# Optimization experiments

Hardware: AMD Instinct MI355X
Metric: run time of the kernel (lower is better)

The kernel has to match this reference:

```python
import jax, jax.numpy as jnp
import numpy as np

SCALE = 4
KUP = 5


def conv2d(x, w, b, pad=0):
    # x: (B,C,H,W), w: (O,I,kh,kw)
    y = jax.lax.conv_general_dilated(x, w, (1, 1), [(pad, pad), (pad, pad)],
                                     dimension_numbers=('NCHW', 'OIHW', 'NCHW'))
    return y + b[None, :, None, None]


def unfold(x, k):
    # torch F.unfold equivalent: (B,C,H,W) -> (B,C,k*k,H,W), channel-major patch order
    p = jax.lax.conv_general_dilated_patches(x, (k, k), (1, 1), [(k // 2, k // 2), (k // 2, k // 2)])
    B, _, H, W = p.shape
    return p.reshape(B, -1, k * k, H, W)


def layernorm(x, g, b, eps=1e-5):
    m = jnp.mean(x, -1, keepdims=True)
    v = jnp.mean((x - m) ** 2, -1, keepdims=True)
    return (x - m) * jax.lax.rsqrt(v + eps) * g + b


def sim(q, k):
    # q: (B,sH,sW,E) high-res queries, k: (B,H,W,E) low-res keys
    B, H, W, C = k.shape
    s, ku = SCALE, KUP
    q6 = q.reshape(B, H, s, W, s, C)
    kunf = unfold(jnp.transpose(k, (0, 3, 1, 2)), ku)  # (B,E,ku^2,H,W)
    a = jnp.einsum('bhswtc,bcphw->bhswtp', q6, kunf)
    return a.reshape(B, s * H, s * W, ku * ku)


def atn(attn, x):
    # attn: (B,sH,sW,ku^2), x: (B,H,W,C) low-res values
    B, H, W, C = x.shape
    s, ku = SCALE, KUP
    a6 = attn.reshape(B, H, s, W, s, ku * ku)
    xunf = unfold(jnp.transpose(x, (0, 3, 1, 2)), ku)  # (B,C,ku^2,H,W)
    o = jnp.einsum('bhswtp,bcphw->bhswtc', a6, xunf)
    return o.reshape(B, s * H, s * W, C)


def setup_inputs() -> dict:
    key = jax.random.key(0)
    ks = jax.random.split(key, 40)
    B, C, H, W, yC, E = 2, 64, 128, 128, 3, 64
    sc = 0.05
    def n(i, shape):
        return jax.random.normal(ks[i], shape, jnp.float32) * sc
    return {
        'x': jax.random.normal(ks[0], (B, C, H, W), jnp.float32),
        'y': jax.random.normal(ks[1], (B, yC, H * SCALE, W * SCALE), jnp.float32),
        'gate_w': n(2, (C, C, 1, 1)), 'gate_b': n(3, (C,)),
        'pc1a_w': n(4, (16, yC + C, 1, 1)), 'pc1a_b': n(5, (16,)),
        'pc1b_w': n(6, (16, 16, 5, 5)), 'pc1b_b': n(7, (16,)),
        'spa1_w': n(8, (16, 16, 3, 3)), 'spa1_b': n(9, (16,)),
        'spa2_w': n(10, (16, 16, 3, 3)), 'spa2_b': n(11, (16,)),
        'frq1_w': n(12, (16, 16, 1, 1)), 'frq1_b': n(13, (16,)),
        'frq2_w': n(14, (16, 16, 1, 1)), 'frq2_b': n(15, (16,)),
        'cat_w': n(16, (8, 32, 1, 1)), 'cat_b': n(17, (8,)),
        'ca1_w': n(18, (2, 8, 1, 1)), 'ca1_b': n(19, (2,)),
        'ca2_w': n(20, (8, 2, 1, 1)), 'ca2_b': n(21, (8,)),
        'pc3_w': n(22, (C, 8, 1, 1)), 'pc3_b': n(23, (C,)),
        'lny_g': jnp.ones((C,), jnp.float32), 'lny_b': jnp.zeros((C,), jnp.float32),
        'lnx_g': jnp.ones((C,), jnp.float32), 'lnx_b': jnp.zeros((C,), jnp.float32),
        'q_w': n(24, (E, C)), 'q_b': n(25, (E,)),
        'k_w': n(26, (E, C)), 'k_b': n(27, (E,)),
    }


def reference(x, y, gate_w, gate_b, pc1a_w, pc1a_b, pc1b_w, pc1b_b,
              spa1_w, spa1_b, spa2_w, spa2_b, frq1_w, frq1_b, frq2_w, frq2_b,
              cat_w, cat_b, ca1_w, ca1_b, ca2_w, ca2_b, pc3_w, pc3_b,
              lny_g, lny_b, lnx_g, lnx_b, q_w, q_b, k_w, k_b):
    B, C, H, W = x.shape
    s = SCALE
    up_x = jax.image.resize(x, (B, C, H * s, W * s), 'cubic')
    gate = jax.nn.sigmoid(conv2d(up_x, gate_w, gate_b))
    # pan_conv1: 1x1 then 5x5
    f = conv2d(jnp.concatenate([y, up_x], 1), pc1a_w, pc1a_b)
    f = conv2d(f, pc1b_w, pc1b_b, pad=2)
    # DDNF: spatial branch (residual conv block stand-in) + frequency branch (1x1 stand-in), cat -> 8ch
    spa = f + conv2d(jax.nn.relu(conv2d(f, spa1_w, spa1_b, pad=1)), spa2_w, spa2_b, pad=1)
    frq = conv2d(jax.nn.relu(conv2d(f, frq1_w, frq1_b)), frq2_w, frq2_b)
    f = conv2d(jnp.concatenate([spa, frq], 1), cat_w, cat_b)
    # ChannelAttention(8, reduction=4): SE-style
    pooled = jnp.mean(f, (2, 3), keepdims=True)
    w = jax.nn.sigmoid(conv2d(jax.nn.relu(conv2d(pooled, ca1_w, ca1_b)), ca2_w, ca2_b))
    f = f * w
    enc = conv2d(f, pc3_w, pc3_b)  # (B,C,sH,sW)
    yb = jnp.transpose(enc, (0, 2, 3, 1))
    xb = jnp.transpose(x, (0, 2, 3, 1))
    yn = layernorm(yb, lny_g, lny_b)
    xn = layernorm(xb, lnx_g, lnx_b)
    q = yn @ q_w.T + q_b  # (B,sH,sW,E)
    k = xn @ k_w.T + k_b  # (B,H,W,E)
    attn = jax.nn.softmax(sim(q, k), axis=-1)
    sapa = jnp.transpose(atn(attn, xb), (0, 3, 1, 2))
    final = gate * sapa + (1.0 - gate) * enc
    return (final, sapa, enc)
```

## Files before the change

### kernel.cpp

```cpp
#include <hip/hip_runtime.h>
#include <hip/hip_bf16.h>
#include <math.h>


#define DEVFN static __device__ __forceinline__

DEVFN float keys_w(float d) {
    if (d < 1.f) return ((1.5f * d - 2.5f) * d) * d + 1.f;
    if (d < 2.f) return ((-0.5f * d + 2.5f) * d - 4.f) * d + 2.f;
    return 0.f;
}

DEVFN void bicubic_axis(int o, int n, int idx4[4], float w4[4]) {
    float f = (o + 0.5f) * 0.25f - 0.5f;
    float fb = floorf(f);
    int ib = (int)fb;
    float t = f - fb;
    float ws[4];
    ws[0] = keys_w(1.f + t);
    ws[1] = keys_w(t);
    ws[2] = keys_w(1.f - t);
    ws[3] = keys_w(2.f - t);
    float s = 0.f;
#pragma unroll
    for (int m = 0; m < 4; m++) {
        int ix = ib - 1 + m;
        if (ix < 0 || ix >= n) ws[m] = 0.f;
        s += ws[m];
        idx4[m] = min(max(ix, 0), n - 1);
    }
    float inv = 1.f / s;
#pragma unroll
    for (int m = 0; m < 4; m++) w4[m] = ws[m] * inv;
}

DEVFN float sigm(float v) { return 1.f / (1.f + __expf(-v)); }

DEVFN unsigned short f2bf(float f) {
    __hip_bfloat16 h = __float2bfloat16(f);
    unsigned short u;
    __builtin_memcpy(&u, &h, 2);
    return u;
}
DEVFN float bf2f(unsigned short u) {
    union { unsigned int i; float f; } z;
    z.i = ((unsigned int)u) << 16;
    return z.f;
}

__global__ __launch_bounds__(256) void k_prep(const float* __restrict__ w5,
                                              const float* __restrict__ w3a,
                                              const float* __restrict__ w3b,
                                              float* __restrict__ wT5,
                                              float* __restrict__ wT3a,
                                              float* __restrict__ wT3b) {
    int t = blockIdx.x * 256 + threadIdx.x;
    if (t < 6400) {
        int tap = t >> 8, ic = (t >> 4) & 15, oc = t & 15;
        wT5[t] = w5[(oc * 16 + ic) * 25 + tap];
    }
    if (t < 2304) {
        int tap = t >> 8, ic = (t >> 4) & 15, oc = t & 15;
        wT3a[t] = w3a[(oc * 16 + ic) * 9 + tap];
        wT3b[t] = w3b[(oc * 16 + ic) * 9 + tap];
    }
}

__global__ __launch_bounds__(256) void k_low(const float* __restrict__ x,
                                             const float* __restrict__ gw, const float* __restrict__ gb,
                                             const float* __restrict__ pw,
                                             const float* __restrict__ lg, const float* __restrict__ lb,
                                             const float* __restrict__ kw, const float* __restrict__ kbias,
                                             float* __restrict__ kb, float* __restrict__ xb,
                                             float* __restrict__ glo, float* __restrict__ plo) {
    int idx = blockIdx.x * 256 + threadIdx.x;
    int w = idx & 127, h = (idx >> 7) & 127, b = idx >> 14;
    const float* xp = x + (size_t)b * 64 * 16384 + (h << 7) + w;
    float xv[64];
#pragma unroll
    for (int c = 0; c < 64; c++) xv[c] = xp[(size_t)c << 14];
    float4* xbp = (float4*)(xb + (size_t)idx * 64);
#pragma unroll
    for (int c4 = 0; c4 < 16; c4++)
        xbp[c4] = make_float4(xv[4 * c4], xv[4 * c4 + 1], xv[4 * c4 + 2], xv[4 * c4 + 3]);
    float4* gp = (float4*)(glo + (size_t)idx * 64);
#pragma unroll
    for (int e4 = 0; e4 < 16; e4++) {
        float r[4];
#pragma unroll
        for (int u = 0; u < 4; u++) {
            int e = e4 * 4 + u;
            float s = gb[e];
#pragma unroll
            for (int c = 0; c < 64; c++) s = fmaf(xv[c], gw[e * 64 + c], s);
            r[u] = s;
        }
        gp[e4] = make_float4(r[0], r[1], r[2], r[3]);
    }
    float4* pp = (float4*)(plo + (size_t)idx * 16);
#pragma unroll
    for (int e4 = 0; e4 < 4; e4++) {
        float r[4];
#pragma unroll
        for (int u = 0; u < 4; u++) {
            int e = e4 * 4 + u;
            float s = 0.f;
#pragma unroll
            for (int c = 0; c < 64; c++) s = fmaf(xv[c], pw[e * 67 + 3 + c], s);
            r[u] = s;
        }
        pp[e4] = make_float4(r[0], r[1], r[2], r[3]);
    }
    float m = 0.f;
#pragma unroll
    for (int c = 0; c < 64; c++) m += xv[c];
    m *= (1.f / 64.f);
    float var = 0.f;
#pragma unroll
    for (int c = 0; c < 64; c++) {
        float d = xv[c] - m;
        var = fmaf(d, d, var);
    }
    var *= (1.f / 64.f);
    float rstd = rsqrtf(var + 1e-5f);
#pragma unroll
    for (int c = 0; c < 64; c++) xv[c] = (xv[c] - m) * rstd * lg[c] + lb[c];
    float4* kp = (float4*)(kb + (size_t)idx * 64);
#pragma unroll
    for (int e4 = 0; e4 < 16; e4++) {
        float r[4];
#pragma unroll
        for (int u = 0; u < 4; u++) {
            int e = e4 * 4 + u;
            float s = kbias[e];
#pragma unroll
            for (int c = 0; c < 64; c++) s = fmaf(xv[c], kw[e * 64 + c], s);
            r[u] = s;
        }
        kp[e4] = make_float4(r[0], r[1], r[2], r[3]);
    }
}

__global__ __launch_bounds__(256) void k_gp(const float* __restrict__ glo, const float* __restrict__ plo,
                                            const float* __restrict__ y,
                                            const float* __restrict__ paw, const float* __restrict__ pab,
                                            __hip_bfloat16* __restrict__ gate, float* __restrict__ f0) {
    __shared__ float v[68 * 81];
    int bid = blockIdx.x;
    int b = bid >> 10, i = (bid >> 1) & 511, j0 = (bid & 1) << 8;
    int t = threadIdx.x;
    int iy[4];
    float wy[4];
    bicubic_axis(i, 128, iy, wy);
    int c0 = (j0 >> 2) - 2;
    for (int e = t; e < 68 * 80; e += 256) {
        int ch = e % 80, lc = e / 80;
        int gc = c0 + lc;
        float val = 0.f;
        if ((unsigned)gc < 128u) {
            if (ch < 64) {
                val = wy[0] * glo[(size_t)((b * 128 + iy[0]) * 128 + gc) * 64 + ch] +
                      wy[1] * glo[(size_t)((b * 128 + iy[1]) * 128 + gc) * 64 + ch] +
                      wy[2] * glo[(size_t)((b * 128 + iy[2]) * 128 + gc) * 64 + ch] +
                      wy[3] * glo[(size_t)((b * 128 + iy[3]) * 128 + gc) * 64 + ch];
            } else {
                int cc = ch - 64;
                val = wy[0] * plo[(size_t)((b * 128 + iy[0]) * 128 + gc) * 16 + cc] +
                      wy[1] * plo[(size_t)((b * 128 + iy[1]) * 128 + gc) * 16 + cc] +
                      wy[2] * plo[(size_t)((b * 128 + iy[2]) * 128 + gc) * 16 + cc] +
                      wy[3] * plo[(size_t)((b * 128 + iy[3]) * 128 + gc) * 16 + cc];
            }
        }
        v[lc * 81 + ch] = val;
    }
    __syncthreads();
    int j = j0 + t;
    int jx[4];
    float wx[4];
    bicubic_axis(j, 128, jx, wx);
    int lx0 = jx[0] - c0, lx1 = jx[1] - c0, lx2 = jx[2] - c0, lx3 = jx[3] - c0;
    float out[80];
#pragma unroll
    for (int ch = 0; ch < 80; ch++)
        out[ch] = wx[0] * v[lx0 * 81 + ch] + wx[1] * v[lx1 * 81 + ch] +
                  wx[2] * v[lx2 * 81 + ch] + wx[3] * v[lx3 * 81 + ch];
    size_t pxoff = ((size_t)b << 18) + ((size_t)i << 9) + j;
    unsigned int uu[32];
#pragma unroll
    for (int k = 0; k < 32; k++) {
        unsigned short h0 = f2bf(sigm(out[2 * k]));
        unsigned short h1 = f2bf(sigm(out[2 * k + 1]));
        uu[k] = (unsigned int)h0 | ((unsigned int)h1 << 16);
    }
    uint4* gp4 = (uint4*)((unsigned short*)gate + pxoff * 64);
#pragma unroll
    for (int k4 = 0; k4 < 8; k4++)
        gp4[k4] = make_uint4(uu[4 * k4], uu[4 * k4 + 1], uu[4 * k4 + 2], uu[4 * k4 + 3]);
    float yc0 = y[((size_t)(b * 3 + 0) << 18) + ((size_t)i << 9) + j];
    float yc1 = y[((size_t)(b * 3 + 1) << 18) + ((size_t)i << 9) + j];
    float yc2 = y[((size_t)(b * 3 + 2) << 18) + ((size_t)i << 9) + j];
    float4* fp = (float4*)(f0 + pxoff * 16);
#pragma unroll
    for (int e4 = 0; e4 < 4; e4++) {
        float r[4];
#pragma unroll
        for (int u = 0; u < 4; u++) {
            int oc = e4 * 4 + u;
            r[u] = out[64 + oc] + pab[oc] + yc0 * paw[oc * 67 + 0] + yc1 * paw[oc * 67 + 1] + yc2 * paw[oc * 67 + 2];
        }
        fp[e4] = make_float4(r[0], r[1], r[2], r[3]);
    }
}

__global__ __launch_bounds__(256) void k_conv5(const float* __restrict__ fin,
                                               const float* __restrict__ wT,
                                               const float* __restrict__ bias,
                                               float* __restrict__ fout) {
    __shared__ float lds[8 * 68 * 20];
    int tid = threadIdx.x;
    int bid = blockIdx.x;
    int seg = bid & 7, it = (bid >> 3) & 127, b = bid >> 10;
    int i0 = it * 4, j0 = seg * 64;
    for (int s = tid; s < 2176; s += 256) {
        int part = s & 3, px = s >> 2;
        int row = px / 68, col = px - row * 68;
        int gi = i0 - 2 + row, gj = j0 - 2 + col;
        float4 v = make_float4(0.f, 0.f, 0.f, 0.f);
        if ((unsigned)gi < 512u && (unsigned)gj < 512u)
            v = *(const float4*)(fin + (((size_t)b << 18) + ((size_t)gi << 9) + gj) * 16 + part * 4);
        *(float4*)(&lds[(row * 68 + col) * 20 + part * 4]) = v;
    }
    __syncthreads();
    int tx = tid & 63, ty = tid >> 6;
    float acc[16];
#pragma unroll
    for (int oc = 0; oc < 16; oc++) acc[oc] = bias[oc];
#pragma unroll
    for (int ky = 0; ky < 5; ky++) {
#pragma unroll
        for (int kx = 0; kx < 5; kx++) {
            const float* p = &lds[((ty + ky) * 68 + tx + kx) * 20];
            float vv[16];
            *(float4*)(vv + 0) = *(const float4*)(p + 0);
            *(float4*)(vv + 4) = *(const float4*)(p + 4);
            *(float4*)(vv + 8) = *(const float4*)(p + 8);
            *(float4*)(vv + 12) = *(const float4*)(p + 12);
            const float* wp = wT + (ky * 5 + kx) * 256;
#pragma unroll
            for (int ic = 0; ic < 16; ic++) {
                float v = vv[ic];
#pragma unroll
                for (int oc = 0; oc < 16; oc++)
                    acc[oc] = fmaf(v, wp[ic * 16 + oc], acc[oc]);
            }
        }
    }
    int i = i0 + ty, j = j0 + tx;
    float4* op = (float4*)(fout + (((size_t)b << 18) + ((size_t)i << 9) + j) * 16);
    op[0] = make_float4(acc[0], acc[1], acc[2], acc[3]);
    op[1] = make_float4(acc[4], acc[5], acc[6], acc[7]);
    op[2] = make_float4(acc[8], acc[9], acc[10], acc[11]);
    op[3] = make_float4(acc[12], acc[13], acc[14], acc[15]);
}

__global__ __launch_bounds__(256) void k_conv3r(const float* __restrict__ fin,
                                                const float* __restrict__ wT,
                                                const float* __restrict__ bias,
                                                float* __restrict__ fout) {
    __shared__ float lds[6 * 66 * 20];
    int tid = threadIdx.x;
    int bid = blockIdx.x;
    int seg = bid & 7, it = (bid >> 3) & 127, b = bid >> 10;
    int i0 = it * 4, j0 = seg * 64;
    for (int s = tid; s < 1584; s += 256) {
        int part = s & 3, px = s >> 2;
        int row = px / 66, col = px - row * 66;
        int gi = i0 - 1 + row, gj = j0 - 1 + col;
        float4 v = make_float4(0.f, 0.f, 0.f, 0.f);
        if ((unsigned)gi < 512u && (unsigned)gj < 512u)
            v = *(const float4*)(fin + (((size_t)b << 18) + ((size_t)gi << 9) + gj) * 16 + part * 4);
        *(float4*)(&lds[(row * 66 + col) * 20 + part * 4]) = v;
    }
    __syncthreads();
    int tx = tid & 63, ty = tid >> 6;
    float acc[16];
#pragma unroll
    for (int oc = 0; oc < 16; oc++) acc[oc] = bias[oc];
#pragma unroll
    for (int ky = 0; ky < 3; ky++) {
#pragma unroll
        for (int kx = 0; kx < 3; kx++) {
            const float* p = &lds[((ty + ky) * 66 + tx + kx) * 20];
            float vv[16];
            *(float4*)(vv + 0) = *(const float4*)(p + 0);
            *(float4*)(vv + 4) = *(const float4*)(p + 4);
            *(float4*)(vv + 8) = *(const float4*)(p + 8);
            *(float4*)(vv + 12) = *(const float4*)(p + 12);
            const float* wp = wT + (ky * 3 + kx) * 256;
#pragma unroll
            for (int ic = 0; ic < 16; ic++) {
                float v = vv[ic];
#pragma unroll
                for (int oc = 0; oc < 16; oc++)
                    acc[oc] = fmaf(v, wp[ic * 16 + oc], acc[oc]);
            }
        }
    }
    int i = i0 + ty, j = j0 + tx;
    float4* op = (float4*)(fout + (((size_t)b << 18) + ((size_t)i << 9) + j) * 16);
    op[0] = make_float4(fmaxf(acc[0], 0.f), fmaxf(acc[1], 0.f), fmaxf(acc[2], 0.f), fmaxf(acc[3], 0.f));
    op[1] = make_float4(fmaxf(acc[4], 0.f), fmaxf(acc[5], 0.f), fmaxf(acc[6], 0.f), fmaxf(acc[7], 0.f));
    op[2] = make_float4(fmaxf(acc[8], 0.f), fmaxf(acc[9], 0.f), fmaxf(acc[10], 0.f), fmaxf(acc[11], 0.f));
    op[3] = make_float4(fmaxf(acc[12], 0.f), fmaxf(acc[13], 0.f), fmaxf(acc[14], 0.f), fmaxf(acc[15], 0.f));
}

__global__ __launch_bounds__(256) void k_tail(const float* __restrict__ f1,
                                              const float* __restrict__ t,
                                              const float* __restrict__ wT2,
                                              const float* __restrict__ s2b,
                                              const float* __restrict__ q1w, const float* __restrict__ q1b,
                                              const float* __restrict__ q2w, const float* __restrict__ q2b,
                                              const float* __restrict__ cw_, const float* __restrict__ cb_,
                                              float* __restrict__ f8) {
    __shared__ float lds[6 * 66 * 20];
    int tid = threadIdx.x;
    int bid = blockIdx.x;
    int seg = bid & 7, it = (bid >> 3) & 127, b = bid >> 10;
    int i0 = it * 4, j0 = seg * 64;
    for (int s = tid; s < 1584; s += 256) {
        int part = s & 3, px = s >> 2;
        int row = px / 66, col = px - row * 66;
        int gi = i0 - 1 + row, gj = j0 - 1 + col;
        float4 v = make_float4(0.f, 0.f, 0.f, 0.f);
        if ((unsigned)gi < 512u && (unsigned)gj < 512u)
            v = *(const float4*)(t + (((size_t)b << 18) + ((size_t)gi << 9) + gj) * 16 + part * 4);
        *(float4*)(&lds[(row * 66 + col) * 20 + part * 4]) = v;
    }
    __syncthreads();
    int tx = tid & 63, ty = tid >> 6;
    int i = i0 + ty, j = j0 + tx;
    float sp[16];
#pragma unroll
    for (int oc = 0; oc < 16; oc++) sp[oc] = s2b[oc];
#pragma unroll
    for (int ky = 0; ky < 3; ky++) {
#pragma unroll
        for (int kx = 0; kx < 3; kx++) {
            const float* p = &lds[((ty + ky) * 66 + tx + kx) * 20];
            float vv[16];
            *(float4*)(vv + 0) = *(const float4*)(p + 0);
            *(float4*)(vv + 4) = *(const float4*)(p + 4);
            *(float4*)(vv + 8) = *(const float4*)(p + 8);
            *(float4*)(vv + 12) = *(const float4*)(p + 12);
            const float* wp = wT2 + (ky * 3 + kx) * 256;
#pragma unroll
            for (int ic = 0; ic < 16; ic++) {
                float v = vv[ic];
#pragma unroll
                for (int oc = 0; oc < 16; oc++)
                    sp[oc] = fmaf(v, wp[ic * 16 + oc], sp[oc]);
            }
        }
    }
    float fv[16];
    const float4* f1p = (const float4*)(f1 + (((size_t)b << 18) + ((size_t)i << 9) + j) * 16);
    *(float4*)(fv + 0) = f1p[0];
    *(float4*)(fv + 4) = f1p[1];
    *(float4*)(fv + 8) = f1p[2];
    *(float4*)(fv + 12) = f1p[3];
#pragma unroll
    for (int c = 0; c < 16; c++) sp[c] += fv[c];
    float mid[16];
#pragma unroll
    for (int r = 0; r < 16; r++) {
        float m = q1b[r];
#pragma unroll
        for (int c = 0; c < 16; c++) m = fmaf(fv[c], q1w[r * 16 + c], m);
        mid[r] = fmaxf(m, 0.f);
    }
    float fo[16];
#pragma unroll
    for (int r = 0; r < 16; r++) {
        float m = q2b[r];
#pragma unroll
        for (int c = 0; c < 16; c++) m = fmaf(mid[c], q2w[r * 16 + c], m);
        fo[r] = m;
    }
    float r8[8];
#pragma unroll
    for (int o = 0; o < 8; o++) {
        float a = cb_[o];
#pragma unroll
        for (int c = 0; c < 16; c++) a = fmaf(sp[c], cw_[o * 32 + c], a);
#pragma unroll
        for (int c = 0; c < 16; c++) a = fmaf(fo[c], cw_[o * 32 + 16 + c], a);
        r8[o] = a;
    }
    float4* op = (float4*)(f8 + (((size_t)b << 18) + ((size_t)i << 9) + j) * 8);
    op[0] = make_float4(r8[0], r8[1], r8[2], r8[3]);
    op[1] = make_float4(r8[4], r8[5], r8[6], r8[7]);
}

__global__ __launch_bounds__(256) void k_pool(const float* __restrict__ f8, float* __restrict__ partials) {
    int b = blockIdx.x >> 4, blk = blockIdx.x & 15;
    const float4* fp = (const float4*)(f8 + (((size_t)b) << 18) * 8);
    float acc[8];
#pragma unroll
    for (int c = 0; c < 8; c++) acc[c] = 0.f;
    int p0 = blk * 16384;
    for (int p = p0 + threadIdx.x; p < p0 + 16384; p += 256) {
        float4 a0 = fp[p * 2], a1 = fp[p * 2 + 1];
        acc[0] += a0.x; acc[1] += a0.y; acc[2] += a0.z; acc[3] += a0.w;
        acc[4] += a1.x; acc[5] += a1.y; acc[6] += a1.z; acc[7] += a1.w;
    }
#pragma unroll
    for (int off = 32; off; off >>= 1) {
#pragma unroll
        for (int c = 0; c < 8; c++) acc[c] += __shfl_down(acc[c], off, 64);
    }
    __shared__ float ls[4][8];
    int lane = threadIdx.x & 63, wv = threadIdx.x >> 6;
    if (lane == 0) {
#pragma unroll
        for (int c = 0; c < 8; c++) ls[wv][c] = acc[c];
    }
    __syncthreads();
    if (threadIdx.x < 8) {
        float s = ls[0][threadIdx.x] + ls[1][threadIdx.x] + ls[2][threadIdx.x] + ls[3][threadIdx.x];
        partials[(b * 8 + threadIdx.x) * 16 + blk] = s;
    }
}

__global__ void k_se(const float* __restrict__ partials,
                     const float* __restrict__ w1, const float* __restrict__ b1,
                     const float* __restrict__ w2, const float* __restrict__ b2,
                     float* __restrict__ cw) {
    int b = threadIdx.x;
    if (b >= 2) return;
    float pooled[8];
#pragma unroll
    for (int c = 0; c < 8; c++) {
        float s = 0.f;
#pragma unroll
        for (int k = 0; k < 16; k++) s += partials[(b * 8 + c) * 16 + k];
        pooled[c] = s * (1.f / 262144.f);
    }
    float mid[2];
#pragma unroll
    for (int r = 0; r < 2; r++) {
        float m = b1[r];
#pragma unroll
        for (int c = 0; c < 8; c++) m = fmaf(w1[r * 8 + c], pooled[c], m);
        mid[r] = fmaxf(m, 0.f);
    }
#pragma unroll
    for (int c = 0; c < 8; c++) {
        float v = b2[c] + w2[c * 2 + 0] * mid[0] + w2[c * 2 + 1] * mid[1];
        cw[b * 8 + c] = 1.f / (1.f + __expf(-v));
    }
}

__global__ __launch_bounds__(256) void k_pc3(const float* __restrict__ f8, const float* __restrict__ cw,
                                             const float* __restrict__ w, const float* __restrict__ bias,
                                             const float* __restrict__ lg, const float* __restrict__ lb,
                                             const float* __restrict__ qw, const float* __restrict__ qbias,
                                             float* __restrict__ enc, unsigned short* __restrict__ qbuf) {
    int idx = blockIdx.x * 256 + threadIdx.x;
    int b = idx >> 18;
    size_t hi = (size_t)idx & 262143;
    const float4* fp = (const float4*)(f8 + (size_t)idx * 8);
    float4 a0 = fp[0], a1 = fp[1];
    float v[8] = {a0.x, a0.y, a0.z, a0.w, a1.x, a1.y, a1.z, a1.w};
#pragma unroll
    for (int c = 0; c < 8; c++) v[c] *= cw[b * 8 + c];
    float yn[64];
#pragma unroll
    for (int oc = 0; oc < 64; oc++) {
        float a = bias[oc];
#pragma unroll
        for (int c = 0; c < 8; c++) a = fmaf(v[c], w[oc * 8 + c], a);
        yn[oc] = a;
        enc[((size_t)(b * 64 + oc) << 18) + hi] = a;
    }
    float m = 0.f;
#pragma unroll
    for (int c = 0; c < 64; c++) m += yn[c];
    m *= (1.f / 64.f);
    float var = 0.f;
#pragma unroll
    for (int c = 0; c < 64; c++) {
        float d = yn[c] - m;
        var = fmaf(d, d, var);
    }
    var *= (1.f / 64.f);
    float rstd = rsqrtf(var + 1e-5f);
#pragma unroll
    for (int c = 0; c < 64; c++) yn[c] = (yn[c] - m) * rstd * lg[c] + lb[c];
    unsigned short* qp = qbuf + (size_t)idx * 64;
    for (int e0 = 0; e0 < 64; e0 += 8) {
        float qv[8];
#pragma unroll
        for (int u = 0; u < 8; u++) {
            float s = qbias[e0 + u];
#pragma unroll
            for (int c = 0; c < 64; c++) s = fmaf(yn[c], qw[(e0 + u) * 64 + c], s);
            qv[u] = s;
        }
        unsigned int pk[4];
#pragma unroll
        for (int u = 0; u < 4; u++)
            pk[u] = (unsigned int)f2bf(qv[2 * u]) | ((unsigned int)f2bf(qv[2 * u + 1]) << 16);
        *(uint4*)(qp + e0) = make_uint4(pk[0], pk[1], pk[2], pk[3]);
    }
}

__global__ __launch_bounds__(256) void k_attn(const float* __restrict__ enc,
                                              const __hip_bfloat16* __restrict__ gate,
                                              const unsigned short* __restrict__ qb,
                                              const float* __restrict__ kb, const float* __restrict__ xbv,
                                              float* __restrict__ sapa, float* __restrict__ fin) {
    __shared__ float tile[100 * 68];
    int tid = threadIdx.x;
    int bid = blockIdx.x;
    int b = bid >> 12, i = (bid >> 3) & 511, jb = bid & 7;
    int j0 = jb << 6;
    int h = i >> 2;
    int wbase = j0 >> 2;
    int cg = tid & 3, px = tid >> 2;
    int j = j0 + px;
    size_t pix = ((size_t)b << 18) + ((size_t)i << 9) + j;
    const uint4* qp = (const uint4*)(qb + pix * 64 + cg * 16);
    uint4 q0 = qp[0], q1 = qp[1];
    unsigned int qu[8] = {q0.x, q0.y, q0.z, q0.w, q1.x, q1.y, q1.z, q1.w};
    float q[16];
#pragma unroll
    for (int k = 0; k < 8; k++) {
        q[2 * k] = bf2f((unsigned short)(qu[k] & 0xffff));
        q[2 * k + 1] = bf2f((unsigned short)(qu[k] >> 16));
    }
    for (int s = tid; s < 1600; s += 256) {
        int p = s >> 4, e4 = s & 15;
        int row = p / 20, col = p - row * 20;
        int hh = h - 2 + row, ww = wbase - 2 + col;
        float4 val = make_float4(0.f, 0.f, 0.f, 0.f);
        if ((unsigned)hh < 128u && (unsigned)ww < 128u)
            val = ((const float4*)(kb + (size_t)((b * 128 + hh) * 128 + ww) * 64))[e4];
        *(float4*)(tile + p * 68 + e4 * 4) = val;
    }
    __syncthreads();
    int wl = px >> 2;
    float a[25];
#pragma unroll
    for (int dy = 0; dy < 5; dy++) {
#pragma unroll
        for (int dx = 0; dx < 5; dx++) {
            int lp = dy * 20 + wl + dx;
            const float4* kp = (const float4*)(tile + lp * 68 + cg * 16);
            float s = 0.f;
#pragma unroll
            for (int e4 = 0; e4 < 4; e4++) {
                float4 kv = kp[e4];
                s = fmaf(q[4 * e4 + 0], kv.x, s);
                s = fmaf(q[4 * e4 + 1], kv.y, s);
                s = fmaf(q[4 * e4 + 2], kv.z, s);
                s = fmaf(q[4 * e4 + 3], kv.w, s);
            }
            a[dy * 5 + dx] = s;
        }
    }
#pragma unroll
    for (int p = 0; p < 25; p++) {
        a[p] += __shfl_xor(a[p], 1, 4);
        a[p] += __shfl_xor(a[p], 2, 4);
    }
    float mx = a[0];
#pragma unroll
    for (int p = 1; p < 25; p++) mx = fmaxf(mx, a[p]);
    float Z = 0.f;
#pragma unroll
    for (int p = 0; p < 25; p++) {
        a[p] = __expf(a[p] - mx);
        Z += a[p];
    }
    float invZ = 1.f / Z;
    __syncthreads();
    for (int s = tid; s < 1600; s += 256) {
        int p = s >> 4, e4 = s & 15;
        int row = p / 20, col = p - row * 20;
        int hh = h - 2 + row, ww = wbase - 2 + col;
        float4 val = make_float4(0.f, 0.f, 0.f, 0.f);
        if ((unsigned)hh < 128u && (unsigned)ww < 128u)
            val = ((const float4*)(xbv + (size_t)((b * 128 + hh) * 128 + ww) * 64))[e4];
        *(float4*)(tile + p * 68 + e4 * 4) = val;
    }
    __syncthreads();
    float o[16];
#pragma unroll
    for (int k = 0; k < 16; k++) o[k] = 0.f;
#pragma unroll
    for (int dy = 0; dy < 5; dy++) {
#pragma unroll
        for (int dx = 0; dx < 5; dx++) {
            float wp = a[dy * 5 + dx];
            int lp = dy * 20 + wl + dx;
            const float4* xp = (const float4*)(tile + lp * 68 + cg * 16);
#pragma unroll
            for (int e4 = 0; e4 < 4; e4++) {
                float4 xv = xp[e4];
                o[4 * e4 + 0] = fmaf(wp, xv.x, o[4 * e4 + 0]);
                o[4 * e4 + 1] = fmaf(wp, xv.y, o[4 * e4 + 1]);
                o[4 * e4 + 2] = fmaf(wp, xv.z, o[4 * e4 + 2]);
                o[4 * e4 + 3] = fmaf(wp, xv.w, o[4 * e4 + 3]);
            }
        }
    }
    const uint4* gp4 = (const uint4*)((const unsigned short*)gate + pix * 64 + cg * 16);
    uint4 g0 = gp4[0], g1 = gp4[1];
    unsigned int gu[8] = {g0.x, g0.y, g0.z, g0.w, g1.x, g1.y, g1.z, g1.w};
    size_t obase = ((size_t)b << 24) + ((size_t)i << 9) + j;
    const float* ep = enc + obase;
#pragma unroll
    for (int cc = 0; cc < 16; cc++) {
        int c = cg * 16 + cc;
        size_t oidx = obase + ((size_t)c << 18);
        float sv = o[cc] * invZ;
        sapa[oidx] = sv;
        unsigned int wbits = gu[cc >> 1];
        unsigned short hb = (cc & 1) ? (unsigned short)(wbits >> 16) : (unsigned short)(wbits & 0xffff);
        float gv = bf2f(hb);
        float ev = ep[(size_t)c << 18];
        fin[oidx] = gv * sv + (1.f - gv) * ev;
    }
}

extern "C" void kernel_launch(void* const* d_in, const int* in_sizes, int n_in,
                              void* d_out, int out_size, void* d_ws, size_t ws_size,
                              hipStream_t stream) {
    const float* x = (const float*)d_in[0];
    const float* y = (const float*)d_in[1];
    const float* gate_w = (const float*)d_in[2];
    const float* gate_b = (const float*)d_in[3];
    const float* pc1a_w = (const float*)d_in[4];
    const float* pc1a_b = (const float*)d_in[5];
    const float* pc1b_w = (const float*)d_in[6];
    const float* pc1b_b = (const float*)d_in[7];
    const float* spa1_w = (const float*)d_in[8];
    const float* spa1_b = (const float*)d_in[9];
    const float* spa2_w = (const float*)d_in[10];
    const float* spa2_b = (const float*)d_in[11];
    const float* frq1_w = (const float*)d_in[12];
    const float* frq1_b = (const float*)d_in[13];
    const float* frq2_w = (const float*)d_in[14];
    const float* frq2_b = (const float*)d_in[15];
    const float* cat_w = (const float*)d_in[16];
    const float* cat_b = (const float*)d_in[17];
    const float* ca1_w = (const float*)d_in[18];
    const float* ca1_b = (const float*)d_in[19];
    const float* ca2_w = (const float*)d_in[20];
    const float* ca2_b = (const float*)d_in[21];
    const float* pc3_w = (const float*)d_in[22];
    const float* pc3_b = (const float*)d_in[23];
    const float* lny_g = (const float*)d_in[24];
    const float* lny_b = (const float*)d_in[25];
    const float* lnx_g = (const float*)d_in[26];
    const float* lnx_b = (const float*)d_in[27];
    const float* q_w = (const float*)d_in[28];
    const float* q_b = (const float*)d_in[29];
    const float* k_w = (const float*)d_in[30];
    const float* k_b = (const float*)d_in[31];

    float* out = (float*)d_out;
    float* finalp = out;
    float* sapap = out + 33554432;
    float* encp = out + 67108864;

    char* ws = (char*)d_ws;
    __hip_bfloat16* gate = (__hip_bfloat16*)ws;
    float* f0 = (float*)(ws + 67108864);
    float* f1 = (float*)(ws + 100663296);
    float* f8 = (float*)(ws + 134217728);
    float* kbuf = (float*)(ws + 150994944);
    float* xbuf = (float*)(ws + 159383552);
    float* partials = (float*)(ws + 167772160);
    float* cw = (float*)(ws + 167773184);
    float* wT5 = (float*)(ws + 167773248);
    float* wT3a = (float*)(ws + 167798848);
    float* wT3b = (float*)(ws + 167808064);
    float* glo = f1;
    float* plo = f1 + 2097152;
    float* tbuf = f0;
    unsigned short* qbuf = (unsigned short*)(ws + 67108864);

    dim3 blk(256);
    dim3 gridHi(2048);
    dim3 gridConv(2048);

    k_prep<<<dim3(25), blk, 0, stream>>>(pc1b_w, spa1_w, spa2_w, wT5, wT3a, wT3b);
    k_low<<<dim3(128), blk, 0, stream>>>(x, gate_w, gate_b, pc1a_w, lnx_g, lnx_b, k_w, k_b,
                                         kbuf, xbuf, glo, plo);
    k_gp<<<gridHi, blk, 0, stream>>>(glo, plo, y, pc1a_w, pc1a_b, gate, f0);
    k_conv5<<<gridConv, blk, 0, stream>>>(f0, wT5, pc1b_b, f1);
    k_conv3r<<<gridConv, blk, 0, stream>>>(f1, wT3a, spa1_b, tbuf);
    k_tail<<<gridConv, blk, 0, stream>>>(f1, tbuf, wT3b, spa2_b, frq1_w, frq1_b,
                                         frq2_w, frq2_b, cat_w, cat_b, f8);
    k_pool<<<dim3(32), blk, 0, stream>>>(f8, partials);
    k_se<<<dim3(1), dim3(64), 0, stream>>>(partials, ca1_w, ca1_b, ca2_w, ca2_b, cw);
    k_pc3<<<gridHi, blk, 0, stream>>>(f8, cw, pc3_w, pc3_b, lny_g, lny_b, q_w, q_b, encp, qbuf);
    k_attn<<<dim3(8192), blk, 0, stream>>>(encp, gate, qbuf, kbuf, xbuf, sapap, finalp);
}
```

Before: 846.7 us.

## Reuse staged K/V tiles across four high-res rows in attention kernel

Each attention block now processes the four high-res rows that share one low-res row. It loads the 5x20 K and X neighbourhood tiles into two separate shared buffers once, which removes the second tile reload and barrier and quarters the number of blocks and tile loads. Output stores become nontemporal to avoid polluting cache. In exchange, shared memory per block doubles (about 54KB), which may lower occupancy, and there are fewer blocks with more serial work each.

New measurement: 1.160 ms. 37.0% more time.

```diff
diff --git a/kernel.cpp b/kernel.cpp
--- a/kernel.cpp
+++ b/kernel.cpp
@@ -519,117 +519,115 @@
                                               const unsigned short* __restrict__ qb,
                                               const float* __restrict__ kb, const float* __restrict__ xbv,
                                               float* __restrict__ sapa, float* __restrict__ fin) {
-    __shared__ float tile[100 * 68];
+    __shared__ float kT[100 * 68];
+    __shared__ float xT[100 * 68];
     int tid = threadIdx.x;
     int bid = blockIdx.x;
-    int b = bid >> 12, i = (bid >> 3) & 511, jb = bid & 7;
+    int b = bid >> 10, hb = (bid >> 3) & 127, jb = bid & 7;
     int j0 = jb << 6;
-    int h = i >> 2;
     int wbase = j0 >> 2;
     int cg = tid & 3, px = tid >> 2;
     int j = j0 + px;
-    size_t pix = ((size_t)b << 18) + ((size_t)i << 9) + j;
-    const uint4* qp = (const uint4*)(qb + pix * 64 + cg * 16);
-    uint4 q0 = qp[0], q1 = qp[1];
-    unsigned int qu[8] = {q0.x, q0.y, q0.z, q0.w, q1.x, q1.y, q1.z, q1.w};
-    float q[16];
-#pragma unroll
-    for (int k = 0; k < 8; k++) {
-        q[2 * k] = bf2f((unsigned short)(qu[k] & 0xffff));
-        q[2 * k + 1] = bf2f((unsigned short)(qu[k] >> 16));
-    }
-    for (int s = tid; s < 1600; s += 256) {
-        int p = s >> 4, e4 = s & 15;
+    int wl = px >> 2;
+    for (int s = tid; s < 3200; s += 256) {
+        int buf = s >= 1600;
+        int r = s - buf * 1600;
+        int p = r >> 4, e4 = r & 15;
         int row = p / 20, col = p - row * 20;
-        int hh = h - 2 + row, ww = wbase - 2 + col;
+        int hh = hb - 2 + row, ww = wbase - 2 + col;
         float4 val = make_float4(0.f, 0.f, 0.f, 0.f);
-        if ((unsigned)hh < 128u && (unsigned)ww < 128u)
-            val = ((const float4*)(kb + (size_t)((b * 128 + hh) * 128 + ww) * 64))[e4];
-        *(float4*)(tile + p * 68 + e4 * 4) = val;
+        if ((unsigned)hh < 128u && (unsigned)ww < 128u) {
+            const float* src = buf ? xbv : kb;
+            val = ((const float4*)(src + (size_t)((b * 128 + hh) * 128 + ww) * 64))[e4];
+        }
+        float* dst = buf ? xT : kT;
+        *(float4*)(dst + p * 68 + e4 * 4) = val;
     }
     __syncthreads();
-    int wl = px >> 2;
-    float a[25];
-#pragma unroll
-    for (int dy = 0; dy < 5; dy++) {
-#pragma unroll
-        for (int dx = 0; dx < 5; dx++) {
-            int lp = dy * 20 + wl + dx;
-            const float4* kp = (const float4*)(tile + lp * 68 + cg * 16);
-            float s = 0.f;
-#pragma unroll
-            for (int e4 = 0; e4 < 4; e4++) {
-                float4 kv = kp[e4];
-                s = fmaf(q[4 * e4 + 0], kv.x, s);
-                s = fmaf(q[4 * e4 + 1], kv.y, s);
-                s = fmaf(q[4 * e4 + 2], kv.z, s);
-                s = fmaf(q[4 * e4 + 3], kv.w, s);
+#pragma unroll 1
+    for (int r = 0; r < 4; r++) {
+        int i = (hb << 2) + r;
+        size_t pix = ((size_t)b << 18) + ((size_t)i << 9) + j;
+        const uint4* qp = (const uint4*)(qb + pix * 64 + cg * 16);
+        uint4 q0 = qp[0], q1 = qp[1];
+        unsigned int qu[8] = {q0.x, q0.y, q0.z, q0.w, q1.x, q1.y, q1.z, q1.w};
+        float q[16];
+#pragma unroll
+        for (int k = 0; k < 8; k++) {
+            q[2 * k] = bf2f((unsigned short)(qu[k] & 0xffff));
+            q[2 * k + 1] = bf2f((unsigned short)(qu[k] >> 16));
+        }
+        float a[25];
+#pragma unroll
+        for (int dy = 0; dy < 5; dy++) {
+#pragma unroll
+            for (int dx = 0; dx < 5; dx++) {
+                int lp = dy * 20 + wl + dx;
+                const float4* kp = (const float4*)(kT + lp * 68 + cg * 16);
+                float s = 0.f;
+#pragma unroll
+                for (int e4 = 0; e4 < 4; e4++) {
+                    float4 kv = kp[e4];
+                    s = fmaf(q[4 * e4 + 0], kv.x, s);
+                    s = fmaf(q[4 * e4 + 1], kv.y, s);
+                    s = fmaf(q[4 * e4 + 2], kv.z, s);
+                    s = fmaf(q[4 * e4 + 3], kv.w, s);
+                }
+                a[dy * 5 + dx] = s;
             }
-            a[dy * 5 + dx] = s;
-        }
-    }
-#pragma unroll
-    for (int p = 0; p < 25; p++) {
-        a[p] += __shfl_xor(a[p], 1, 4);
-        a[p] += __shfl_xor(a[p], 2, 4);
-    }
-    float mx = a[0];
-#pragma unroll
-    for (int p = 1; p < 25; p++) mx = fmaxf(mx, a[p]);
-    float Z = 0.f;
-#pragma unroll
-    for (int p = 0; p < 25; p++) {
-        a[p] = __expf(a[p] - mx);
-        Z += a[p];
-    }
-    float invZ = 1.f / Z;
-    __syncthreads();
-    for (int s = tid; s < 1600; s += 256) {
-        int p = s >> 4, e4 = s & 15;
-        int row = p / 20, col = p - row * 20;
-        int hh = h - 2 + row, ww = wbase - 2 + col;
-        float4 val = make_float4(0.f, 0.f, 0.f, 0.f);
-        if ((unsigned)hh < 128u && (unsigned)ww < 128u)
-            val = ((const float4*)(xbv + (size_t)((b * 128 + hh) * 128 + ww) * 64))[e4];
-        *(float4*)(tile + p * 68 + e4 * 4) = val;
-    }
-    __syncthreads();
-    float o[16];
-#pragma unroll
-    for (int k = 0; k < 16; k++) o[k] = 0.f;
-#pragma unroll
-    for (int dy = 0; dy < 5; dy++) {
-#pragma unroll
-        for (int dx = 0; dx < 5; dx++) {
-            float wp = a[dy * 5 + dx];
-            int lp = dy * 20 + wl + dx;
-            const float4* xp = (const float4*)(tile + lp * 68 + cg * 16);
-#pragma unroll
-            for (int e4 = 0; e4 < 4; e4++) {
-                float4 xv = xp[e4];
-                o[4 * e4 + 0] = fmaf(wp, xv.x, o[4 * e4 + 0]);
-                o[4 * e4 + 1] = fmaf(wp, xv.y, o[4 * e4 + 1]);
-                o[4 * e4 + 2] = fmaf(wp, xv.z, o[4 * e4 + 2]);
-                o[4 * e4 + 3] = fmaf(wp, xv.w, o[4 * e4 + 3]);
+        }
+#pragma unroll
+        for (int p = 0; p < 25; p++) {
+            a[p] += __shfl_xor(a[p], 1, 4);
+            a[p] += __shfl_xor(a[p], 2, 4);
+        }
+        float mx = a[0];
+#pragma unroll
+        for (int p = 1; p < 25; p++) mx = fmaxf(mx, a[p]);
+        float Z = 0.f;
+#pragma unroll
+        for (int p = 0; p < 25; p++) {
+            a[p] = __expf(a[p] - mx);
+            Z += a[p];
+        }
+        float invZ = 1.f / Z;
+        float o[16];
+#pragma unroll
+        for (int k = 0; k < 16; k++) o[k] = 0.f;
+#pragma unroll
+        for (int dy = 0; dy < 5; dy++) {
+#pragma unroll
+            for (int dx = 0; dx < 5; dx++) {
+                float wp = a[dy * 5 + dx];
+                int lp = dy * 20 + wl + dx;
+                const float4* xp = (const float4*)(xT + lp * 68 + cg * 16);
+#pragma unroll
+                for (int e4 = 0; e4 < 4; e4++) {
+                    float4 xv = xp[e4];
+                    o[4 * e4 + 0] = fmaf(wp, xv.x, o[4 * e4 + 0]);
+                    o[4 * e4 + 1] = fmaf(wp, xv.y, o[4 * e4 + 1]);
+                    o[4 * e4 + 2] = fmaf(wp, xv.z, o[4 * e4 + 2]);
+                    o[4 * e4 + 3] = fmaf(wp, xv.w, o[4 * e4 + 3]);
+                }
             }
         }
-    }
-    const uint4* gp4 = (const uint4*)((const unsigned short*)gate + pix * 64 + cg * 16);
-    uint4 g0 = gp4[0], g1 = gp4[1];
-    unsigned int gu[8] = {g0.x, g0.y, g0.z, g0.w, g1.x, g1.y, g1.z, g1.w};
-    size_t obase = ((size_t)b << 24) + ((size_t)i << 9) + j;
-    const float* ep = enc + obase;
-#pragma unroll
-    for (int cc = 0; cc < 16; cc++) {
-        int c = cg * 16 + cc;
-        size_t oidx = obase + ((size_t)c << 18);
-        float sv = o[cc] * invZ;
-        sapa[oidx] = sv;
-        unsigned int wbits = gu[cc >> 1];
-        unsigned short hb = (cc & 1) ? (unsigned short)(wbits >> 16) : (unsigned short)(wbits & 0xffff);
-        float gv = bf2f(hb);
-        float ev = ep[(size_t)c << 18];
-        fin[oidx] = gv * sv + (1.f - gv) * ev;
+        const uint4* gp4 = (const uint4*)((const unsigned short*)gate + pix * 64 + cg * 16);
+        uint4 g0 = gp4[0], g1 = gp4[1];
+        unsigned int gu[8] = {g0.x, g0.y, g0.z, g0.w, g1.x, g1.y, g1.z, g1.w};
+        size_t obase = ((size_t)b << 24) + ((size_t)i << 9) + j;
+        const float* ep = enc + obase;
+#pragma unroll
+        for (int cc = 0; cc < 16; cc++) {
+            int c = cg * 16 + cc;
+            size_t oidx = obase + ((size_t)c << 18);
+            float sv = o[cc] * invZ;
+            __builtin_nontemporal_store(sv, &sapa[oidx]);
+            unsigned int wbits = gu[cc >> 1];
+            unsigned short hb2 = (cc & 1) ? (unsigned short)(wbits >> 16) : (unsigned short)(wbits & 0xffff);
+            float gv = bf2f(hb2);
+            float ev = ep[(size_t)c << 18];
+            __builtin_nontemporal_store(gv * sv + (1.f - gv) * ev, &fin[oidx]);
+        }
     }
 }
 
@@ -706,5 +704,5 @@
     k_pool<<<dim3(32), blk, 0, stream>>>(f8, partials);
     k_se<<<dim3(1), dim3(64), 0, stream>>>(partials, ca1_w, ca1_b, ca2_w, ca2_b, cw);
     k_pc3<<<gridHi, blk, 0, stream>>>(f8, cw, pc3_w, pc3_b, lny_g, lny_b, q_w, q_b, encp, qbuf);
-    k_attn<<<dim3(8192), blk, 0, stream>>>(encp, gate, qbuf, kbuf, xbuf, sapap, finalp);
-}
+    k_attn<<<dim3(2048), blk, 0, stream>>>(encp, gate, qbuf, kbuf, xbuf, sapap, finalp);
+}
```
